# Kernel tuning notes

Measured on AMD Instinct MI355X. Metric: run time of the kernel, lower is better.

## Reference

```python
import jax, jax.numpy as jnp
import numpy as np

GRID_RES = 32      # sparse_grid_dim
GRID_DIM = 8       # dense cells per sparse block side
NUM_EMB = 12000    # number of sparse blocks
EMB_DIM = 1
N_POINTS = 2000000
N_CELLS = GRID_RES * GRID_DIM  # 256^3 virtual dense grid over [-1,1]^3


def _interp_point(pos, embeddings, block_table):
    """Trilinear interp of a sparse block-grid at one world point in [-1,1]^3.

    embeddings: [NUM_EMB, GRID_DIM^3, EMB_DIM]
    block_table: [GRID_RES]^3 int32, block index or -1 if unallocated.
    Returns (emb [EMB_DIM], valid_all bool).
    """
    xc = (pos + 1.0) * 0.5 * (N_CELLS - 1)            # world -> cell coords
    base = jnp.clip(jnp.floor(xc), 0.0, N_CELLS - 2).astype(jnp.int32)
    frac = xc - base.astype(xc.dtype)
    emb = jnp.zeros((EMB_DIM,), xc.dtype)
    valid_all = jnp.bool_(True)
    for dx in (0, 1):
        for dy in (0, 1):
            for dz in (0, 1):
                corner = base + jnp.array([dx, dy, dz], jnp.int32)
                blk = corner // GRID_DIM                 # sparse block coord
                loc = corner % GRID_DIM                  # local cell coord
                bidx = block_table[blk[0], blk[1], blk[2]]
                valid = bidx >= 0
                li = (loc[0] * GRID_DIM + loc[1]) * GRID_DIM + loc[2]
                e = embeddings[jnp.maximum(bidx, 0), li]
                wx = frac[0] if dx else 1.0 - frac[0]
                wy = frac[1] if dy else 1.0 - frac[1]
                wz = frac[2] if dz else 1.0 - frac[2]
                emb = emb + jnp.where(valid, wx * wy * wz, 0.0) * e
                valid_all = jnp.logical_and(valid_all, valid)
    return emb, valid_all


def setup_inputs() -> dict:
    key = jax.random.key(0)
    k1, k2 = jax.random.split(key, 2)
    positions = jax.random.uniform(k1, (N_POINTS, 3), minval=-1.0, maxval=1.0,
                                   dtype=jnp.float32)
    # original init zeros the embeddings; use small randn for a non-trivial test
    embeddings = 0.1 * jax.random.normal(k2, (NUM_EMB, GRID_DIM ** 3, EMB_DIM),
                                         dtype=jnp.float32)
    # sparse occupancy: NUM_EMB random blocks of the GRID_RES^3 lattice allocated
    rng = np.random.default_rng(0)
    table = -np.ones(GRID_RES ** 3, np.int32)
    table[rng.permutation(GRID_RES ** 3)[:NUM_EMB]] = np.arange(NUM_EMB, dtype=np.int32)
    block_table = jnp.asarray(table.reshape(GRID_RES, GRID_RES, GRID_RES))
    return {"positions": positions, "embeddings": embeddings,
            "block_table": block_table}


@jax.jit
def reference(positions, embeddings, block_table):
    def f(pos):
        e, v = _interp_point(pos, embeddings, block_table)
        return e[0], v
    # value_and_grad mirrors torch.autograd.grad(embedding[...,0], positions)
    (emb, mask), grad_x = jax.vmap(jax.value_and_grad(f, has_aux=True))(positions)
    return emb[:, None], grad_x, mask
```

## Files before the change

### kernel.cpp

```cpp
#include <hip/hip_runtime.h>
#include <hip/hip_bf16.h>

#define GRID_RES 32
#define GRID_DIM 8
#define N_CELLS  256
#define EMB_VOL  512
#define TAB_N    (GRID_RES * GRID_RES * GRID_RES)
#define NPT      4
#define BLOCK    512


__device__ __forceinline__ unsigned bf16rne(float f) {
    unsigned u = __float_as_uint(f);
    return (u + 0x7fffu + ((u >> 16) & 1u)) >> 16;
}

__global__ __launch_bounds__(256) void build_pairs(
    const float* __restrict__ emb, const int* __restrict__ table,
    unsigned* __restrict__ pb)
{
    int tid = blockIdx.x * 256 + threadIdx.x;
    int entry = tid >> 6;
    if (entry >= TAB_N) return;
    int row = tid & 63;
    int b = table[entry];
    if (b < 0) return;
    int BZ = entry & (GRID_RES - 1);
    int zn = (BZ < GRID_RES - 1) ? table[entry + 1] : -1;

    const float* src = emb + (size_t)b * EMB_VOL + row * 8;
    float4 a0 = *reinterpret_cast<const float4*>(src);
    float4 a1 = *reinterpret_cast<const float4*>(src + 4);
    float e0=a0.x, e1=a0.y, e2=a0.z, e3=a0.w;
    float e4=a1.x, e5=a1.y, e6=a1.z, e7=a1.w;
    float e8 = (zn >= 0) ? emb[(size_t)zn * EMB_VOL + row * 8] : 0.0f;

    unsigned o0 = bf16rne(e0) | (bf16rne(e1) << 16);
    unsigned o1 = bf16rne(e2) | (bf16rne(e3) << 16);
    unsigned o2 = bf16rne(e4) | (bf16rne(e5) << 16);
    unsigned o3 = bf16rne(e6) | (bf16rne(e7) << 16);
    unsigned o4 = bf16rne(e1) | (bf16rne(e2) << 16);
    unsigned o5 = bf16rne(e3) | (bf16rne(e4) << 16);
    unsigned o6 = bf16rne(e5) | (bf16rne(e6) << 16);
    unsigned o7 = bf16rne(e7) | (bf16rne(e8) << 16);

    uint4* dst = reinterpret_cast<uint4*>(pb + (size_t)b * EMB_VOL + row * 8);
    dst[0] = make_uint4(o0, o1, o2, o3);
    dst[1] = make_uint4(o4, o5, o6, o7);
}

__global__ __launch_bounds__(BLOCK) void interp_pairs(
    const float* __restrict__ positions,
    const float* __restrict__ emb,
    const int*   __restrict__ table,
    const unsigned* __restrict__ pb,
    float* __restrict__ out, int n)
{
    __shared__ short stab[TAB_N];
    {
        const int4* t4 = reinterpret_cast<const int4*>(table);
        for (int k = threadIdx.x; k < TAB_N / 4; k += BLOCK) {
            int4 v = t4[k];
            short4 s;
            s.x = (short)v.x; s.y = (short)v.y; s.z = (short)v.z; s.w = (short)v.w;
            *reinterpret_cast<short4*>(&stab[4 * k]) = s;
        }
    }
    __syncthreads();

    int nq = (n + NPT - 1) / NPT;
    int stride = gridDim.x * BLOCK;
    for (int q = blockIdx.x * BLOCK + threadIdx.x; q < nq; q += stride) {
        int i0 = q * NPT;
        bool full = (i0 + NPT <= n);

        float px[NPT], py[NPT], pz[NPT];
        if (full) {
            const float4* p4 = reinterpret_cast<const float4*>(positions + 3 * (size_t)i0);
            float4 A = p4[0], B = p4[1], C = p4[2];
            px[0]=A.x; py[0]=A.y; pz[0]=A.z;
            px[1]=A.w; py[1]=B.x; pz[1]=B.y;
            px[2]=B.z; py[2]=B.w; pz[2]=C.x;
            px[3]=C.y; py[3]=C.z; pz[3]=C.w;
        } else {
#pragma unroll
            for (int p = 0; p < NPT; ++p) {
                int ip = min(i0 + p, n - 1);
                px[p] = positions[3 * ip + 0];
                py[p] = positions[3 * ip + 1];
                pz[p] = positions[3 * ip + 2];
            }
        }

        float wA[NPT][3], wB[NPT][3];
        int tb[NPT][4], tb1[NPT][4];
        unsigned lx4[NPT];
        int lzv[NPT];
        unsigned uu[NPT][4];

#pragma unroll
        for (int p = 0; p < NPT; ++p) {
            float xc[3];
            xc[0] = (px[p] + 1.0f) * 0.5f * (float)(N_CELLS - 1);
            xc[1] = (py[p] + 1.0f) * 0.5f * (float)(N_CELLS - 1);
            xc[2] = (pz[p] + 1.0f) * 0.5f * (float)(N_CELLS - 1);
            int base[3];
#pragma unroll
            for (int a = 0; a < 3; ++a) {
                float bf = fminf(fmaxf(floorf(xc[a]), 0.0f), (float)(N_CELLS - 2));
                float fr = xc[a] - bf;
                wA[p][a] = 1.0f - fr;
                wB[p][a] = fr;
                base[a] = (int)bf;
            }
            int bx = base[0], by = base[1], bz = base[2];
            lzv[p] = bz & 7;
            int bzs0 = bz >> 3, bzs1 = (bz + 1) >> 3;
            unsigned pk = 0;
#pragma unroll
            for (int c = 0; c < 4; ++c) {
                int dx = c >> 1, dy = c & 1;
                int cx = bx + dx, cy = by + dy;
                int tbase = ((cx >> 3) * GRID_RES + (cy >> 3)) * GRID_RES;
                tb [p][c] = stab[tbase + bzs0];
                tb1[p][c] = stab[tbase + bzs1];
                unsigned lxly = (unsigned)((cx & 7) * 8 + (cy & 7));
                pk |= lxly << (8 * c);
            }
            lx4[p] = pk;
        }

#pragma unroll
        for (int p = 0; p < NPT; ++p) {
            int lz = lzv[p];
            int zoff = (lz & 1) ? 4 + (lz >> 1) : (lz >> 1);
#pragma unroll
            for (int c = 0; c < 4; ++c) {
                int b = tb[p][c] > 0 ? tb[p][c] : 0;
                int lxly = (lx4[p] >> (8 * c)) & 0xff;
                uu[p][c] = pb[(size_t)b * EMB_VOL + lxly * 8 + zoff];
            }
        }

        const float scale = 0.5f * (float)(N_CELLS - 1);
        float acc[NPT], gxv[NPT], gyv[NPT], gzv[NPT], mk[NPT];

#pragma unroll
        for (int p = 0; p < NPT; ++p) {
            float wz0 = wA[p][2], wz1 = wB[p][2];
            float a = 0.0f, gx = 0.0f, gy = 0.0f, gz = 0.0f;
            bool vall = true;
#pragma unroll
            for (int c = 0; c < 4; ++c) {
                int dx = c >> 1, dy = c & 1;
                bool v0 = tb [p][c] >= 0;
                bool v1 = tb1[p][c] >= 0;
                vall = vall && v0 && v1;
                unsigned u = uu[p][c];
                float e0 = v0 ? __uint_as_float(u << 16) : 0.0f;
                float e1 = v0 ? __uint_as_float(u & 0xffff0000u) : 0.0f;
                if (!v0 && v1) {
                    int lxly = (lx4[p] >> (8 * c)) & 0xff;
                    e1 = emb[(size_t)tb1[p][c] * EMB_VOL + lxly * 8];
                }
                float s = wz0 * e0 + wz1 * e1;
                float wx = dx ? wB[p][0] : wA[p][0];
                float wy = dy ? wB[p][1] : wA[p][1];
                float wxy = wx * wy;
                a  += wxy * s;
                gx += dx ? wy * s : -wy * s;
                gy += dy ? wx * s : -wx * s;
                gz += wxy * (e1 - e0);
            }
            acc[p] = a;
            gxv[p] = scale * gx;
            gyv[p] = scale * gy;
            gzv[p] = scale * gz;
            mk[p]  = vall ? 1.0f : 0.0f;
        }

        float* out_emb  = out;
        float* out_grad = out + (size_t)n;
        float* out_mask = out + 4 * (size_t)n;

        if (full) {
            *reinterpret_cast<float4*>(out_emb + i0) =
                make_float4(acc[0], acc[1], acc[2], acc[3]);
            float4* g4 = reinterpret_cast<float4*>(out_grad + 3 * (size_t)i0);
            g4[0] = make_float4(gxv[0], gyv[0], gzv[0], gxv[1]);
            g4[1] = make_float4(gyv[1], gzv[1], gxv[2], gyv[2]);
            g4[2] = make_float4(gzv[2], gxv[3], gyv[3], gzv[3]);
            *reinterpret_cast<float4*>(out_mask + i0) =
                make_float4(mk[0], mk[1], mk[2], mk[3]);
        } else {
#pragma unroll
            for (int p = 0; p < NPT; ++p) {
                int ip = i0 + p;
                if (ip < n) {
                    out_emb[ip]          = acc[p];
                    out_grad[3 * ip + 0] = gxv[p];
                    out_grad[3 * ip + 1] = gyv[p];
                    out_grad[3 * ip + 2] = gzv[p];
                    out_mask[ip]         = mk[p];
                }
            }
        }
    }
}

__global__ __launch_bounds__(BLOCK) void neural_poisson_interp(
    const float* __restrict__ positions,
    const float* __restrict__ embeddings,
    const int*   __restrict__ block_table,
    float* __restrict__ out, int n)
{
    __shared__ short stab[TAB_N];
    {
        const int4* t4 = reinterpret_cast<const int4*>(block_table);
        for (int k = threadIdx.x; k < TAB_N / 4; k += BLOCK) {
            int4 v = t4[k];
            short4 s;
            s.x = (short)v.x; s.y = (short)v.y; s.z = (short)v.z; s.w = (short)v.w;
            *reinterpret_cast<short4*>(&stab[4 * k]) = s;
        }
    }
    __syncthreads();

    int t = blockIdx.x * blockDim.x + threadIdx.x;
    int i0 = t * NPT;
    if (i0 >= n) return;
    bool full = (i0 + NPT <= n);

    float px[NPT], py[NPT], pz[NPT];
    if (full) {
        const float4* p4 = reinterpret_cast<const float4*>(positions + 3 * (size_t)i0);
        float4 A = p4[0], B = p4[1], C = p4[2];
        px[0]=A.x; py[0]=A.y; pz[0]=A.z;
        px[1]=A.w; py[1]=B.x; pz[1]=B.y;
        px[2]=B.z; py[2]=B.w; pz[2]=C.x;
        px[3]=C.y; py[3]=C.z; pz[3]=C.w;
    } else {
#pragma unroll
        for (int p = 0; p < NPT; ++p) {
            int ip = min(i0 + p, n - 1);
            px[p] = positions[3 * ip + 0];
            py[p] = positions[3 * ip + 1];
            pz[p] = positions[3 * ip + 2];
        }
    }

    float wA[NPT][3], wB[NPT][3];
    int bidx[NPT][8];
    int li[NPT][8];
#pragma unroll
    for (int p = 0; p < NPT; ++p) {
        float xc[3];
        xc[0] = (px[p] + 1.0f) * 0.5f * 255.0f;
        xc[1] = (py[p] + 1.0f) * 0.5f * 255.0f;
        xc[2] = (pz[p] + 1.0f) * 0.5f * 255.0f;
        int base[3];
#pragma unroll
        for (int a = 0; a < 3; ++a) {
            float bf = fminf(fmaxf(floorf(xc[a]), 0.0f), 254.0f);
            float fr = xc[a] - bf;
            wA[p][a] = 1.0f - fr;
            wB[p][a] = fr;
            base[a] = (int)bf;
        }
#pragma unroll
        for (int c = 0; c < 8; ++c) {
            int dx = (c >> 2) & 1, dy = (c >> 1) & 1, dz = c & 1;
            int cx = base[0] + dx, cy = base[1] + dy, cz = base[2] + dz;
            bidx[p][c] = stab[((cx >> 3) * GRID_RES + (cy >> 3)) * GRID_RES + (cz >> 3)];
            li[p][c] = ((cx & 7) * GRID_DIM + (cy & 7)) * GRID_DIM + (cz & 7);
        }
    }
    float e[NPT][8];
#pragma unroll
    for (int p = 0; p < NPT; ++p)
#pragma unroll
        for (int c = 0; c < 8; ++c) {
            int b = bidx[p][c] > 0 ? bidx[p][c] : 0;
            e[p][c] = embeddings[b * EMB_VOL + li[p][c]];
        }
    const float scale = 127.5f;
    float acc[NPT], gxv[NPT], gyv[NPT], gzv[NPT], mk[NPT];
#pragma unroll
    for (int p = 0; p < NPT; ++p) {
        float a = 0.0f, gx = 0.0f, gy = 0.0f, gz = 0.0f;
        bool vall = true;
#pragma unroll
        for (int c = 0; c < 8; ++c) {
            int dx = (c >> 2) & 1, dy = (c >> 1) & 1, dz = c & 1;
            bool valid = bidx[p][c] >= 0;
            vall = vall && valid;
            float ev = valid ? e[p][c] : 0.0f;
            float wx = dx ? wB[p][0] : wA[p][0];
            float wy = dy ? wB[p][1] : wA[p][1];
            float wz = dz ? wB[p][2] : wA[p][2];
            a += wx * wy * wz * ev;
            float tgx = wy * wz * ev;
            float tgy = wx * wz * ev;
            float tgz = wx * wy * ev;
            gx += dx ? tgx : -tgx;
            gy += dy ? tgy : -tgy;
            gz += dz ? tgz : -tgz;
        }
        acc[p] = a; gxv[p] = scale * gx; gyv[p] = scale * gy; gzv[p] = scale * gz;
        mk[p] = vall ? 1.0f : 0.0f;
    }
    float* out_emb  = out;
    float* out_grad = out + (size_t)n;
    float* out_mask = out + 4 * (size_t)n;
    if (full) {
        *reinterpret_cast<float4*>(out_emb + i0) =
            make_float4(acc[0], acc[1], acc[2], acc[3]);
        float4* g4 = reinterpret_cast<float4*>(out_grad + 3 * (size_t)i0);
        g4[0] = make_float4(gxv[0], gyv[0], gzv[0], gxv[1]);
        g4[1] = make_float4(gyv[1], gzv[1], gxv[2], gyv[2]);
        g4[2] = make_float4(gzv[2], gxv[3], gyv[3], gzv[3]);
        *reinterpret_cast<float4*>(out_mask + i0) =
            make_float4(mk[0], mk[1], mk[2], mk[3]);
    } else {
#pragma unroll
        for (int p = 0; p < NPT; ++p) {
            int ip = i0 + p;
            if (ip < n) {
                out_emb[ip] = acc[p];
                out_grad[3 * ip + 0] = gxv[p];
                out_grad[3 * ip + 1] = gyv[p];
                out_grad[3 * ip + 2] = gzv[p];
                out_mask[ip] = mk[p];
            }
        }
    }
}

extern "C" void kernel_launch(void* const* d_in, const int* in_sizes, int n_in,
                              void* d_out, int out_size, void* d_ws, size_t ws_size,
                              hipStream_t stream) {
    const float* positions   = (const float*)d_in[0];
    const float* embeddings  = (const float*)d_in[1];
    const int*   block_table = (const int*)d_in[2];

    int n = in_sizes[0] / 3;
    int nblocks = in_sizes[1] / EMB_VOL;
    size_t pair_bytes = (size_t)nblocks * EMB_VOL * sizeof(unsigned);
    float* out = (float*)d_out;

    if (ws_size >= pair_bytes) {
        unsigned* pb = (unsigned*)d_ws;
        build_pairs<<<(TAB_N * 64 + 255) / 256, 256, 0, stream>>>(
            embeddings, block_table, pb);
        int nq = (n + NPT - 1) / NPT;
        int grid = 512;
        int maxg = (nq + BLOCK - 1) / BLOCK;
        if (grid > maxg) grid = maxg;
        interp_pairs<<<grid, BLOCK, 0, stream>>>(
            positions, embeddings, block_table, pb, out, n);
    } else {
        int nthreads = (n + NPT - 1) / NPT;
        int grid = (nthreads + BLOCK - 1) / BLOCK;
        neural_poisson_interp<<<grid, BLOCK, 0, stream>>>(
            positions, embeddings, block_table, out, n);
    }
}
```

Before: 136.8 us.

## Precompute per-cell 8-corner bf16 cubes so each point does one 16-byte gather

New measurement: 156.8 us. +14.6%, slower.

```diff
diff --git a/kernel.cpp b/kernel.cpp
--- a/kernel.cpp
+++ b/kernel.cpp
@@ -9,51 +9,65 @@
 #define NPT      4
 #define BLOCK    512
 
-
 __device__ __forceinline__ unsigned bf16rne(float f) {
     unsigned u = __float_as_uint(f);
     return (u + 0x7fffu + ((u >> 16) & 1u)) >> 16;
 }
-
-__global__ __launch_bounds__(256) void build_pairs(
+__device__ __forceinline__ float bf16lo(unsigned u) { return __uint_as_float(u << 16); }
+__device__ __forceinline__ float bf16hi(unsigned u) { return __uint_as_float(u & 0xffff0000u); }
+
+__global__ __launch_bounds__(256) void build_cubes(
     const float* __restrict__ emb, const int* __restrict__ table,
-    unsigned* __restrict__ pb)
+    uint4* __restrict__ cube)
 {
     int tid = blockIdx.x * 256 + threadIdx.x;
     int entry = tid >> 6;
     if (entry >= TAB_N) return;
-    int row = tid & 63;
     int b = table[entry];
     if (b < 0) return;
-    int BZ = entry & (GRID_RES - 1);
-    int zn = (BZ < GRID_RES - 1) ? table[entry + 1] : -1;
-
-    const float* src = emb + (size_t)b * EMB_VOL + row * 8;
-    float4 a0 = *reinterpret_cast<const float4*>(src);
-    float4 a1 = *reinterpret_cast<const float4*>(src + 4);
-    float e0=a0.x, e1=a0.y, e2=a0.z, e3=a0.w;
-    float e4=a1.x, e5=a1.y, e6=a1.z, e7=a1.w;
-    float e8 = (zn >= 0) ? emb[(size_t)zn * EMB_VOL + row * 8] : 0.0f;
-
-    unsigned o0 = bf16rne(e0) | (bf16rne(e1) << 16);
-    unsigned o1 = bf16rne(e2) | (bf16rne(e3) << 16);
-    unsigned o2 = bf16rne(e4) | (bf16rne(e5) << 16);
-    unsigned o3 = bf16rne(e6) | (bf16rne(e7) << 16);
-    unsigned o4 = bf16rne(e1) | (bf16rne(e2) << 16);
-    unsigned o5 = bf16rne(e3) | (bf16rne(e4) << 16);
-    unsigned o6 = bf16rne(e5) | (bf16rne(e6) << 16);
-    unsigned o7 = bf16rne(e7) | (bf16rne(e8) << 16);
-
-    uint4* dst = reinterpret_cast<uint4*>(pb + (size_t)b * EMB_VOL + row * 8);
-    dst[0] = make_uint4(o0, o1, o2, o3);
-    dst[1] = make_uint4(o4, o5, o6, o7);
-}
-
-__global__ __launch_bounds__(BLOCK) void interp_pairs(
+    int r  = tid & 63;
+    int lx = r >> 3, ly = r & 7;
+    int BX = entry >> 10, BY = (entry >> 5) & 31, BZ = entry & 31;
+
+    float v[4][9];
+#pragma unroll
+    for (int i = 0; i < 4; ++i) {
+        int ax = lx + (i >> 1), ay = ly + (i & 1);
+        int sx = ax >> 3, sy = ay >> 3;
+        bool ok = (BX + sx < GRID_RES) && (BY + sy < GRID_RES);
+        int ex = entry + sx * 1024 + sy * 32;
+        int rb = ok ? table[ex] : -1;
+        int lxl = ax & 7, lyl = ay & 7;
+        if (rb >= 0) {
+            const float* src = emb + (size_t)rb * EMB_VOL + (lxl * 8 + lyl) * 8;
+            float4 a0 = *reinterpret_cast<const float4*>(src);
+            float4 a1 = *reinterpret_cast<const float4*>(src + 4);
+            v[i][0]=a0.x; v[i][1]=a0.y; v[i][2]=a0.z; v[i][3]=a0.w;
+            v[i][4]=a1.x; v[i][5]=a1.y; v[i][6]=a1.z; v[i][7]=a1.w;
+        } else {
+#pragma unroll
+            for (int z = 0; z < 8; ++z) v[i][z] = 0.0f;
+        }
+        int zb = (ok && (BZ + 1 < GRID_RES)) ? table[ex + 1] : -1;
+        v[i][8] = (zb >= 0) ? emb[(size_t)zb * EMB_VOL + (lxl * 8 + lyl) * 8] : 0.0f;
+    }
+
+    uint4* dst = cube + ((size_t)b * EMB_VOL + (lx * 8 + ly) * 8);
+#pragma unroll
+    for (int lz = 0; lz < 8; ++lz) {
+        unsigned u0 = bf16rne(v[0][lz]) | (bf16rne(v[0][lz + 1]) << 16);
+        unsigned u1 = bf16rne(v[1][lz]) | (bf16rne(v[1][lz + 1]) << 16);
+        unsigned u2 = bf16rne(v[2][lz]) | (bf16rne(v[2][lz + 1]) << 16);
+        unsigned u3 = bf16rne(v[3][lz]) | (bf16rne(v[3][lz + 1]) << 16);
+        dst[lz] = make_uint4(u0, u1, u2, u3);
+    }
+}
+
+__global__ __launch_bounds__(BLOCK) void interp_cubes(
     const float* __restrict__ positions,
     const float* __restrict__ emb,
     const int*   __restrict__ table,
-    const unsigned* __restrict__ pb,
+    const uint4* __restrict__ cube,
     float* __restrict__ out, int n)
 {
     __shared__ short stab[TAB_N];
@@ -93,10 +107,9 @@
         }
 
         float wA[NPT][3], wB[NPT][3];
-        int tb[NPT][4], tb1[NPT][4];
-        unsigned lx4[NPT];
-        int lzv[NPT];
-        unsigned uu[NPT][4];
+        int bxv[NPT], byv[NPT], bzv[NPT];
+        short tc[NPT][8];
+        uint4 cu[NPT];
 
 #pragma unroll
         for (int p = 0; p < NPT; ++p) {
@@ -114,32 +127,26 @@
                 base[a] = (int)bf;
             }
             int bx = base[0], by = base[1], bz = base[2];
-            lzv[p] = bz & 7;
-            int bzs0 = bz >> 3, bzs1 = (bz + 1) >> 3;
-            unsigned pk = 0;
-#pragma unroll
-            for (int c = 0; c < 4; ++c) {
-                int dx = c >> 1, dy = c & 1;
-                int cx = bx + dx, cy = by + dy;
-                int tbase = ((cx >> 3) * GRID_RES + (cy >> 3)) * GRID_RES;
-                tb [p][c] = stab[tbase + bzs0];
-                tb1[p][c] = stab[tbase + bzs1];
-                unsigned lxly = (unsigned)((cx & 7) * 8 + (cy & 7));
-                pk |= lxly << (8 * c);
-            }
-            lx4[p] = pk;
-        }
-
-#pragma unroll
-        for (int p = 0; p < NPT; ++p) {
-            int lz = lzv[p];
-            int zoff = (lz & 1) ? 4 + (lz >> 1) : (lz >> 1);
-#pragma unroll
-            for (int c = 0; c < 4; ++c) {
-                int b = tb[p][c] > 0 ? tb[p][c] : 0;
-                int lxly = (lx4[p] >> (8 * c)) & 0xff;
-                uu[p][c] = pb[(size_t)b * EMB_VOL + lxly * 8 + zoff];
-            }
+            bxv[p] = bx; byv[p] = by; bzv[p] = bz;
+            int eidx = ((bx >> 3) * GRID_RES + (by >> 3)) * GRID_RES + (bz >> 3);
+            int ox = ((bx & 7) == 7) ? (GRID_RES * GRID_RES) : 0;
+            int oy = ((by & 7) == 7) ? GRID_RES : 0;
+            int oz = ((bz & 7) == 7) ? 1 : 0;
+            tc[p][0] = stab[eidx];
+            tc[p][1] = stab[eidx + oz];
+            tc[p][2] = stab[eidx + oy];
+            tc[p][3] = stab[eidx + oy + oz];
+            tc[p][4] = stab[eidx + ox];
+            tc[p][5] = stab[eidx + ox + oz];
+            tc[p][6] = stab[eidx + ox + oy];
+            tc[p][7] = stab[eidx + ox + oy + oz];
+        }
+
+#pragma unroll
+        for (int p = 0; p < NPT; ++p) {
+            int b = tc[p][0] > 0 ? tc[p][0] : 0;
+            int cell = ((bxv[p] & 7) * 8 + (byv[p] & 7)) * 8 + (bzv[p] & 7);
+            cu[p] = cube[(size_t)b * EMB_VOL + cell];
         }
 
         const float scale = 0.5f * (float)(N_CELLS - 1);
@@ -147,22 +154,35 @@
 
 #pragma unroll
         for (int p = 0; p < NPT; ++p) {
+            float e[4][2];
+            e[0][0] = bf16lo(cu[p].x); e[0][1] = bf16hi(cu[p].x);
+            e[1][0] = bf16lo(cu[p].y); e[1][1] = bf16hi(cu[p].y);
+            e[2][0] = bf16lo(cu[p].z); e[2][1] = bf16hi(cu[p].z);
+            e[3][0] = bf16lo(cu[p].w); e[3][1] = bf16hi(cu[p].w);
+
+            if (tc[p][0] < 0) {
+#pragma unroll
+                for (int i = 0; i < 4; ++i) { e[i][0] = 0.0f; e[i][1] = 0.0f; }
+#pragma unroll
+                for (int c = 0; c < 8; ++c) {
+                    int dx = c >> 2, dy = (c >> 1) & 1, dz = c & 1;
+                    short t = tc[p][c];
+                    if (t >= 0) {
+                        int cx = bxv[p] + dx, cy = byv[p] + dy, cz = bzv[p] + dz;
+                        int li = ((cx & 7) * 8 + (cy & 7)) * 8 + (cz & 7);
+                        e[dx * 2 + dy][dz] = emb[(size_t)t * EMB_VOL + li];
+                    }
+                }
+            }
+
+            int sgn = tc[p][0] & tc[p][1] & tc[p][2] & tc[p][3] &
+                      tc[p][4] & tc[p][5] & tc[p][6] & tc[p][7];
             float wz0 = wA[p][2], wz1 = wB[p][2];
             float a = 0.0f, gx = 0.0f, gy = 0.0f, gz = 0.0f;
-            bool vall = true;
-#pragma unroll
-            for (int c = 0; c < 4; ++c) {
-                int dx = c >> 1, dy = c & 1;
-                bool v0 = tb [p][c] >= 0;
-                bool v1 = tb1[p][c] >= 0;
-                vall = vall && v0 && v1;
-                unsigned u = uu[p][c];
-                float e0 = v0 ? __uint_as_float(u << 16) : 0.0f;
-                float e1 = v0 ? __uint_as_float(u & 0xffff0000u) : 0.0f;
-                if (!v0 && v1) {
-                    int lxly = (lx4[p] >> (8 * c)) & 0xff;
-                    e1 = emb[(size_t)tb1[p][c] * EMB_VOL + lxly * 8];
-                }
+#pragma unroll
+            for (int i = 0; i < 4; ++i) {
+                int dx = i >> 1, dy = i & 1;
+                float e0 = e[i][0], e1 = e[i][1];
                 float s = wz0 * e0 + wz1 * e1;
                 float wx = dx ? wB[p][0] : wA[p][0];
                 float wy = dy ? wB[p][1] : wA[p][1];
@@ -176,7 +196,7 @@
             gxv[p] = scale * gx;
             gyv[p] = scale * gy;
             gzv[p] = scale * gz;
-            mk[p]  = vall ? 1.0f : 0.0f;
+            mk[p]  = (sgn >= 0) ? 1.0f : 0.0f;
         }
 
         float* out_emb  = out;
@@ -345,19 +365,19 @@
 
     int n = in_sizes[0] / 3;
     int nblocks = in_sizes[1] / EMB_VOL;
-    size_t pair_bytes = (size_t)nblocks * EMB_VOL * sizeof(unsigned);
+    size_t cube_bytes = (size_t)nblocks * EMB_VOL * sizeof(uint4);
     float* out = (float*)d_out;
 
-    if (ws_size >= pair_bytes) {
-        unsigned* pb = (unsigned*)d_ws;
-        build_pairs<<<(TAB_N * 64 + 255) / 256, 256, 0, stream>>>(
-            embeddings, block_table, pb);
+    if (ws_size >= cube_bytes) {
+        uint4* cube = (uint4*)d_ws;
+        build_cubes<<<(TAB_N * 64 + 255) / 256, 256, 0, stream>>>(
+            embeddings, block_table, cube);
         int nq = (n + NPT - 1) / NPT;
         int grid = 512;
         int maxg = (nq + BLOCK - 1) / BLOCK;
         if (grid > maxg) grid = maxg;
-        interp_pairs<<<grid, BLOCK, 0, stream>>>(
-            positions, embeddings, block_table, pb, out, n);
+        interp_cubes<<<grid, BLOCK, 0, stream>>>(
+            positions, embeddings, block_table, cube, out, n);
     } else {
         int nthreads = (n + NPT - 1) / NPT;
         int grid = (nthreads + BLOCK - 1) / BLOCK;
```
